# Optimization experiments

Measured on AMD Instinct MI355X. Metric: run time of the kernel, lower is better.

Reference implementation:

```python
import jax, jax.numpy as jnp
import numpy as np

B, S, D_MODEL = 2, 2048, 1024
H, D = 16, 64
D_INNER = H * D
EPS = 1e-5


def setup_inputs() -> dict:
    key = jax.random.key(0)
    ks = jax.random.split(key, 10)
    sc = 0.02
    return {
        "x": jax.random.normal(ks[0], (B, S, D_MODEL), dtype=jnp.float32),
        "Wq": jax.random.normal(ks[1], (D_MODEL, D_INNER), dtype=jnp.float32) * sc,
        "Wk": jax.random.normal(ks[2], (D_MODEL, D_INNER), dtype=jnp.float32) * sc,
        "Wv": jax.random.normal(ks[3], (D_MODEL, D_INNER), dtype=jnp.float32) * sc,
        "Wg": jax.random.normal(ks[4], (D_MODEL, D_INNER), dtype=jnp.float32) * sc,
        "Wa": jax.random.normal(ks[5], (D_MODEL, H), dtype=jnp.float32) * sc,
        "ba": jax.random.normal(ks[6], (H,), dtype=jnp.float32) * sc,
        "Wo": jax.random.normal(ks[7], (D_INNER, D_MODEL), dtype=jnp.float32) * sc,
        "gn_w": jnp.ones((D_INNER,), dtype=jnp.float32),
        "gn_b": jnp.zeros((D_INNER,), dtype=jnp.float32),
    }


def reference(x, Wq, Wk, Wv, Wg, Wa, ba, Wo, gn_w, gn_b):
    b, s, _ = x.shape
    # projections -> [B,H,S,D]
    q = jax.nn.silu(jnp.einsum('bsm,md->bsd', x, Wq).reshape(b, s, H, D).transpose(0, 2, 1, 3))
    k = jax.nn.silu(jnp.einsum('bsm,md->bsd', x, Wk).reshape(b, s, H, D).transpose(0, 2, 1, 3))
    v = jnp.einsum('bsm,md->bsd', x, Wv).reshape(b, s, H, D).transpose(0, 2, 1, 3)

    # data-dependent log forget gate, per head: [B,H,S]
    log_alpha = -jax.nn.softplus(jnp.einsum('bsm,mh->bsh', x, Wa) + ba)
    cum = jnp.cumsum(log_alpha, axis=1).transpose(0, 2, 1)  # [B,H,S]

    # decay[b,h,i,j] = exp(cum[i] - cum[j]) for j <= i, else 0
    diff = cum[:, :, :, None] - cum[:, :, None, :]  # [B,H,S,S]
    causal = jnp.tril(jnp.ones((s, s), dtype=bool))
    decay = jnp.exp(jnp.where(causal, diff, -jnp.inf))

    attn = jnp.einsum('bhid,bhjd->bhij', q, k) * decay
    o = jnp.einsum('bhij,bhjd->bhid', attn, v)  # [B,H,S,D]
    o = o.transpose(0, 2, 1, 3)  # [B,S,H,D]

    # GroupNorm(H groups) over channels-within-group and spatial dim S
    mean = jnp.mean(o, axis=(1, 3), keepdims=True)          # per (b,h)
    var = jnp.var(o, axis=(1, 3), keepdims=True)
    o = (o - mean) / jnp.sqrt(var + EPS)
    o = o * gn_w.reshape(H, D) + gn_b.reshape(H, D)
    o = o.reshape(b, s, H * D)

    gate = jax.nn.sigmoid(jnp.einsum('bsm,md->bsd', x, Wg))
    return jnp.einsum('bsd,dm->bsm', o * gate, Wo)
```

## Files before the change

### kernel.cpp

```cpp
#include <hip/hip_runtime.h>
#include <math.h>
#include <stdint.h>

typedef __attribute__((ext_vector_type(4))) float f32x4;
typedef __attribute__((ext_vector_type(8))) short bf16x8;

constexpr int NB = 2;
constexpr int NS = 2048;
constexpr int NM = 1024;
constexpr int NH = 16;
constexpr int ND = 64;
constexpr int NDI = 1024;

__device__ __forceinline__ float bf2f(unsigned short u) {
  uint32_t x = ((uint32_t)u) << 16; float f; __builtin_memcpy(&f, &x, 4); return f;
}
__device__ __forceinline__ unsigned short f2bf(float f) {
  uint32_t x; __builtin_memcpy(&x, &f, 4);
  x += 0x7FFFu + ((x >> 16) & 1u);
  return (unsigned short)(x >> 16);
}

__global__ __launch_bounds__(256) void k_prep(const float* __restrict__ x,
    const float* __restrict__ w0, const float* __restrict__ w1,
    const float* __restrict__ w2, const float* __restrict__ w3,
    const float* __restrict__ w4, const float* __restrict__ Wa,
    unsigned short* __restrict__ xb,
    unsigned short* __restrict__ t0, unsigned short* __restrict__ t1,
    unsigned short* __restrict__ t2, unsigned short* __restrict__ t3,
    unsigned short* __restrict__ t4, unsigned short* __restrict__ wa_pad) {
  int bid = blockIdx.x;
  if (bid < 2048) {
    int i = bid * 256 + threadIdx.x;
    const float4* p = (const float4*)(x + (size_t)i * 8);
    float4 a = p[0], b = p[1];
    unsigned short r[8] = {f2bf(a.x), f2bf(a.y), f2bf(a.z), f2bf(a.w),
                           f2bf(b.x), f2bf(b.y), f2bf(b.z), f2bf(b.w)};
    *(uint4*)(xb + (size_t)i * 8) = *(const uint4*)r;
  } else if (bid < 7168) {
    __shared__ float tile[32][33];
    int w = bid - 2048;
    int z = w >> 10, within = w & 1023;
    const float* src = z == 0 ? w0 : z == 1 ? w1 : z == 2 ? w2 : z == 3 ? w3 : w4;
    unsigned short* dst = z == 0 ? t0 : z == 1 ? t1 : z == 2 ? t2 : z == 3 ? t3 : t4;
    int c0 = (within & 31) * 32, r0 = (within >> 5) * 32;
    int tx = threadIdx.x & 31, ty = threadIdx.x >> 5;
    #pragma unroll
    for (int i = 0; i < 4; i++)
      tile[ty + i * 8][tx] = src[(size_t)(r0 + ty + i * 8) * 1024 + c0 + tx];
    __syncthreads();
    #pragma unroll
    for (int i = 0; i < 4; i++)
      dst[(size_t)(c0 + ty + i * 8) * 1024 + r0 + tx] = f2bf(tile[tx][ty + i * 8]);
  } else {
    int idx = (bid - 7168) * 256 + threadIdx.x;
    int h = idx >> 10, k2 = idx & 1023;
    wa_pad[idx] = (h < 16) ? f2bf(Wa[k2 * 16 + h]) : (unsigned short)0;
  }
}

__global__ __launch_bounds__(256) void k_la_gemm(const unsigned short* __restrict__ xb,
    const unsigned short* __restrict__ wa_pad, float* __restrict__ la4) {
  __shared__ unsigned short As[128 * 32];
  __shared__ unsigned short Bs[128 * 32];
  int tid = threadIdx.x;
  int row0 = blockIdx.y * 128;
  int kbeg = blockIdx.x * 256;
  float* Cp = la4 + (size_t)blockIdx.x * (32 * 2048);
  int w = tid >> 6, l = tid & 63;
  int wr = w >> 1, wc = w & 1;
  int lr = l & 15, lk = l >> 4;
  f32x4 acc[4] = {};
  for (int k0 = kbeg; k0 < kbeg + 256; k0 += 32) {
    __syncthreads();
    #pragma unroll
    for (int i = 0; i < 2; i++) {
      int idx = tid + i * 256;
      int r = idx >> 2, c = idx & 3;
      int cs = c ^ ((r >> 1) & 3);
      const unsigned short* srcA = xb + (size_t)(row0 + r) * NM + k0 + cs * 8;
      const unsigned short* srcB = wa_pad + (size_t)r * NM + k0 + cs * 8;
      __builtin_amdgcn_global_load_lds(
          (const __attribute__((address_space(1))) void*)srcA,
          (__attribute__((address_space(3))) void*)((char*)As + (w * 64 + i * 256) * 16),
          16, 0, 0);
      __builtin_amdgcn_global_load_lds(
          (const __attribute__((address_space(1))) void*)srcB,
          (__attribute__((address_space(3))) void*)((char*)Bs + (w * 64 + i * 256) * 16),
          16, 0, 0);
    }
    __syncthreads();
    if (wc == 0) {
      bf16x8 b = *(const bf16x8*)&Bs[lr * 32 + (lk ^ ((lr >> 1) & 3)) * 8];
      #pragma unroll
      for (int m = 0; m < 4; m++) {
        int ra = wr * 64 + m * 16 + lr;
        bf16x8 a = *(const bf16x8*)&As[ra * 32 + (lk ^ ((ra >> 1) & 3)) * 8];
        acc[m] = __builtin_amdgcn_mfma_f32_16x16x32_bf16(a, b, acc[m], 0, 0, 0);
      }
    }
  }
  if (wc == 0) {
    #pragma unroll
    for (int m = 0; m < 4; m++) {
      #pragma unroll
      for (int j = 0; j < 4; j++) {
        int row = row0 + wr * 64 + m * 16 + lk * 4 + j;
        int bb = row >> 11, s = row & 2047;
        Cp[((size_t)(bb * 16 + lr)) * 2048 + s] = acc[m][j];
      }
    }
  }
}

__global__ __launch_bounds__(256) void k_cumsum(const float* __restrict__ la4,
    const float* __restrict__ ba, float* __restrict__ cum,
    float* __restrict__ psum, float* __restrict__ psq) {
  int g = blockIdx.x;
  int h = g & 15;
  if (threadIdx.x == 0) { psum[g] = 0.f; psq[g] = 0.f; }
  float bah = ba[h];
  const float* p0 = la4 + (size_t)g * NS;
  float* out = cum + (size_t)g * NS;
  __shared__ float part[256];
  float v[8]; float sum = 0.f;
  int base = threadIdx.x * 8;
  #pragma unroll
  for (int i = 0; i < 8; i++) {
    int s = base + i;
    float z = p0[s] + p0[65536 + s] + p0[131072 + s] + p0[196608 + s] + bah;
    float sp = fmaxf(z, 0.f) + log1pf(expf(-fabsf(z)));
    v[i] = -sp; sum += v[i];
  }
  part[threadIdx.x] = sum;
  __syncthreads();
  for (int off = 1; off < 256; off <<= 1) {
    float add = (threadIdx.x >= off) ? part[threadIdx.x - off] : 0.f;
    __syncthreads();
    part[threadIdx.x] += add;
    __syncthreads();
  }
  float run = (threadIdx.x > 0) ? part[threadIdx.x - 1] : 0.f;
  #pragma unroll
  for (int i = 0; i < 8; i++) { run += v[i]; out[base + i] = run; }
}

#define LD8(base, r, kc) (*(const bf16x8*)((base) + (size_t)(r) * 128 + ((((kc)) ^ ((r) & 7)) * 16)))

__global__ __launch_bounds__(512, 1) void k_proj8(
    const unsigned short* __restrict__ A,
    const unsigned short* __restrict__ Wcat,
    unsigned short* __restrict__ q, unsigned short* __restrict__ k,
    unsigned short* __restrict__ v, unsigned short* __restrict__ g) {
  __shared__ unsigned short Ab[2][256 * 64];
  __shared__ unsigned short Bb[2][256 * 64];
  int tid = threadIdx.x;
  int bid = blockIdx.x;
  int wg = (bid & 7) * 32 + (bid >> 3);
  int bx = wg & 15, by = wg >> 4;
  int row0 = by * 256, col0 = bx * 256;
  int wid = tid >> 6, lane = tid & 63;
  int WR = wid >> 2, WC = wid & 3;
  int lr = lane & 15, lk = lane >> 4;

  auto stage = [&](int kt, int bi) {
    #pragma unroll
    for (int i = 0; i < 4; i++) {
      int idx = tid + i * 512;
      int r = idx >> 3, c = idx & 7;
      int cs = c ^ (r & 7);
      const unsigned short* srcA = A + (size_t)(row0 + r) * NM + kt * 64 + cs * 8;
      __builtin_amdgcn_global_load_lds(
          (const __attribute__((address_space(1))) void*)srcA,
          (__attribute__((address_space(3))) void*)((char*)&Ab[bi][0] + (wid * 64 + i * 512) * 16),
          16, 0, 0);
      const unsigned short* srcB = Wcat + (size_t)(col0 + r) * NM + kt * 64 + cs * 8;
      __builtin_amdgcn_global_load_lds(
          (const __attribute__((address_space(1))) void*)srcB,
          (__attribute__((address_space(3))) void*)((char*)&Bb[bi][0] + (wid * 64 + i * 512) * 16),
          16, 0, 0);
    }
  };

  stage(0, 0);
  stage(1, 1);

  f32x4 acc[8][4] = {};
  for (int kt = 0; kt < 16; ++kt) {
    int bi = kt & 1;
    if (kt < 15) asm volatile("s_waitcnt vmcnt(8)" ::: "memory");
    else         asm volatile("s_waitcnt vmcnt(0)" ::: "memory");
    __builtin_amdgcn_sched_barrier(0);
    __builtin_amdgcn_s_barrier();

    const char* Ap = (const char*)&Ab[bi][0];
    const char* Bp = (const char*)&Bb[bi][0];
    bf16x8 a[4][2], blo[2][2], bhi[2][2];
    #pragma unroll
    for (int m = 0; m < 4; m++) {
      int r = WR * 128 + m * 16 + lr;
      a[m][0] = LD8(Ap, r, lk); a[m][1] = LD8(Ap, r, lk + 4);
    }
    #pragma unroll
    for (int n = 0; n < 2; n++) {
      int r = WC * 64 + n * 16 + lr;
      blo[n][0] = LD8(Bp, r, lk); blo[n][1] = LD8(Bp, r, lk + 4);
    }
    __builtin_amdgcn_s_setprio(1);
    #pragma unroll
    for (int kk = 0; kk < 2; kk++)
      #pragma unroll
      for (int m = 0; m < 4; m++)
        #pragma unroll
        for (int n = 0; n < 2; n++)
          acc[m][n] = __builtin_amdgcn_mfma_f32_16x16x32_bf16(a[m][kk], blo[n][kk], acc[m][n], 0, 0, 0);
    __builtin_amdgcn_s_setprio(0);
    #pragma unroll
    for (int n = 0; n < 2; n++) {
      int r = WC * 64 + (2 + n) * 16 + lr;
      bhi[n][0] = LD8(Bp, r, lk); bhi[n][1] = LD8(Bp, r, lk + 4);
    }
    __builtin_amdgcn_s_barrier();
    __builtin_amdgcn_s_setprio(1);
    #pragma unroll
    for (int kk = 0; kk < 2; kk++)
      #pragma unroll
      for (int m = 0; m < 4; m++)
        #pragma unroll
        for (int n = 0; n < 2; n++)
          acc[m][2 + n] = __builtin_amdgcn_mfma_f32_16x16x32_bf16(a[m][kk], bhi[n][kk], acc[m][2 + n], 0, 0, 0);
    __builtin_amdgcn_s_setprio(0);
    #pragma unroll
    for (int m = 0; m < 4; m++) {
      int r = WR * 128 + (4 + m) * 16 + lr;
      a[m][0] = LD8(Ap, r, lk); a[m][1] = LD8(Ap, r, lk + 4);
    }
    __builtin_amdgcn_s_barrier();
    __builtin_amdgcn_s_setprio(1);
    #pragma unroll
    for (int kk = 0; kk < 2; kk++)
      #pragma unroll
      for (int m = 0; m < 4; m++)
        #pragma unroll
        for (int n = 0; n < 2; n++)
          acc[4 + m][2 + n] = __builtin_amdgcn_mfma_f32_16x16x32_bf16(a[m][kk], bhi[n][kk], acc[4 + m][2 + n], 0, 0, 0);
    __builtin_amdgcn_s_setprio(0);
    asm volatile("s_waitcnt lgkmcnt(0)" ::: "memory");
    __builtin_amdgcn_sched_barrier(0);
    __builtin_amdgcn_s_barrier();
    if (kt + 2 < 16) stage(kt + 2, bi);
    __builtin_amdgcn_s_setprio(1);
    #pragma unroll
    for (int kk = 0; kk < 2; kk++)
      #pragma unroll
      for (int m = 0; m < 4; m++)
        #pragma unroll
        for (int n = 0; n < 2; n++)
          acc[4 + m][n] = __builtin_amdgcn_mfma_f32_16x16x32_bf16(a[m][kk], blo[n][kk], acc[4 + m][n], 0, 0, 0);
    __builtin_amdgcn_s_setprio(0);
  }

  #pragma unroll
  for (int m = 0; m < 8; m++) {
    #pragma unroll
    for (int n = 0; n < 4; n++) {
      int col = col0 + WC * 64 + n * 16 + lr;
      int zone = col >> 10;
      unsigned short* dst = zone == 0 ? q : zone == 1 ? k : zone == 2 ? v : g;
      int cb = col & 1023;
      #pragma unroll
      for (int j = 0; j < 4; j++) {
        int row = row0 + WR * 128 + m * 16 + lk * 4 + j;
        float val = acc[m][n][j];
        if (zone <= 1) val = val / (1.f + expf(-val));
        else if (zone == 3) val = 1.f / (1.f + expf(-val));
        dst[(size_t)row * 1024 + cb] = f2bf(val);
      }
    }
  }
}

__global__ __launch_bounds__(256) void k_out2(const unsigned short* __restrict__ A,
    const unsigned short* __restrict__ Bt, float* __restrict__ C) {
  __shared__ unsigned short As[2][128 * 64];
  __shared__ unsigned short Bs[2][128 * 64];
  int tid = threadIdx.x;
  int bid = blockIdx.x;
  int wg = (bid & 7) * 32 + (bid >> 3);
  int bx = wg & 7, by = wg >> 3;
  int row0 = by * 128, col0 = bx * 128;
  int w = tid >> 6, l = tid & 63;
  int wr = w >> 1, wc = w & 1;
  int lr = l & 15, lk = l >> 4;

  auto stage = [&](int t, int bi) {
    #pragma unroll
    for (int i = 0; i < 4; i++) {
      int idx = tid + i * 256;
      int r = idx >> 3, c = idx & 7;
      int cs = c ^ (r & 7);
      const unsigned short* srcA = A + (size_t)(row0 + r) * NM + t * 64 + cs * 8;
      __builtin_amdgcn_global_load_lds(
          (const __attribute__((address_space(1))) void*)srcA,
          (__attribute__((address_space(3))) void*)((char*)&As[bi][0] + idx * 16),
          16, 0, 0);
      const unsigned short* srcB = Bt + (size_t)(col0 + r) * NM + t * 64 + cs * 8;
      __builtin_amdgcn_global_load_lds(
          (const __attribute__((address_space(1))) void*)srcB,
          (__attribute__((address_space(3))) void*)((char*)&Bs[bi][0] + idx * 16),
          16, 0, 0);
    }
  };

  stage(0, 0);
  asm volatile("s_waitcnt vmcnt(0)" ::: "memory");
  __builtin_amdgcn_s_barrier();

  f32x4 acc[4][4] = {};
  int cur = 0;
  for (int t = 0; t < 16; ++t) {
    if (t < 15) stage(t + 1, cur ^ 1);
    const char* Ap = (const char*)&As[cur][0];
    const char* Bp = (const char*)&Bs[cur][0];
    bf16x8 a[4][2], b[4][2];
    #pragma unroll
    for (int m = 0; m < 4; m++) {
      int ra = wr * 64 + m * 16 + lr;
      #pragma unroll
      for (int kk = 0; kk < 2; kk++)
        a[m][kk] = *(const bf16x8*)(Ap + ra * 128 + (((kk * 4 + lk) ^ (ra & 7)) * 16));
    }
    #pragma unroll
    for (int n = 0; n < 4; n++) {
      int rb = wc * 64 + n * 16 + lr;
      #pragma unroll
      for (int kk = 0; kk < 2; kk++)
        b[n][kk] = *(const bf16x8*)(Bp + rb * 128 + (((kk * 4 + lk) ^ (rb & 7)) * 16));
    }
    __builtin_amdgcn_s_setprio(1);
    #pragma unroll
    for (int kk = 0; kk < 2; kk++)
      #pragma unroll
      for (int m = 0; m < 4; m++)
        #pragma unroll
        for (int n = 0; n < 4; n++)
          acc[m][n] = __builtin_amdgcn_mfma_f32_16x16x32_bf16(a[m][kk], b[n][kk], acc[m][n], 0, 0, 0);
    __builtin_amdgcn_s_setprio(0);
    asm volatile("s_waitcnt vmcnt(0)" ::: "memory");
    __builtin_amdgcn_s_barrier();
    cur ^= 1;
  }
  #pragma unroll
  for (int m = 0; m < 4; m++)
    #pragma unroll
    for (int n = 0; n < 4; n++)
      #pragma unroll
      for (int j = 0; j < 4; j++) {
        int row = row0 + wr * 64 + m * 16 + lk * 4 + j;
        int col = col0 + wc * 64 + n * 16 + lr;
        C[(size_t)row * NM + col] = acc[m][n][j];
      }
}

__global__ __launch_bounds__(256) void k_attn(const unsigned short* __restrict__ q,
    const unsigned short* __restrict__ kk, const unsigned short* __restrict__ vv,
    const float* __restrict__ cum, unsigned short* __restrict__ o,
    float* __restrict__ psum, float* __restrict__ psq) {
  int it = blockIdx.x, h = blockIdx.y, b = blockIdx.z;
  int i0 = it * 64;
  __shared__ unsigned short Qs[64 * 64];
  __shared__ unsigned short Ks[64 * 64];
  __shared__ unsigned short Ps[64 * 64];
  __shared__ unsigned short Vs[64 * 66];
  __shared__ float ci[64], cj[64];
  __shared__ int jlo_s;
  int tid = threadIdx.x;
  int w = tid >> 6, lane = tid & 63;
  int cl = lane & 15, hi = lane >> 4;
  const size_t hb = (size_t)b * NS * NDI + (size_t)h * ND;
  const float* cumh = cum + (size_t)(b * NH + h) * NS;

  #pragma unroll
  for (int lp = 0; lp < 2; lp++) {
    int idx = tid + lp * 256;
    int r = idx >> 3, cb = (idx & 7) * 16;
    uint4 t = *(const uint4*)(q + hb + (size_t)(i0 + r) * NDI + (cb >> 1));
    *(uint4*)((char*)Qs + r * 128 + (cb ^ ((r & 7) << 4))) = t;
  }
  if (tid < 64) ci[tid] = cumh[i0 + tid];
  if (tid < 64) {
    int jt = tid;
    bool ok = (jt <= it) && (cumh[i0] - cumh[jt * 64 + 63] >= -60.f);
    unsigned long long mask = __ballot(ok);
    if (tid == 0) jlo_s = (int)__builtin_ctzll(mask);
  }
  __syncthreads();
  int jlo = jlo_s;

  int arow = w * 16 + cl;
  int xr = (cl & 7) << 4;
  const char* Qb = (const char*)Qs + arow * 128;
  const char* Pb = (const char*)Ps + arow * 128;
  f32x4 acco[4] = {};

  for (int jt = jlo; jt <= it; jt++) {
    int j0 = jt * 64;
    __syncthreads();
    if (tid < 64) cj[tid] = cumh[j0 + tid];
    __syncthreads();
    #pragma unroll
    for (int lp = 0; lp < 2; lp++) {
      int idx = tid + lp * 256;
      int r = idx >> 3, cb = (idx & 7) * 16;
      uint4 t = *(const uint4*)(kk + hb + (size_t)(j0 + r) * NDI + (cb >> 1));
      *(uint4*)((char*)Ks + r * 128 + (cb ^ ((r & 7) << 4))) = t;
      uint4 tv = *(const uint4*)(vv + hb + (size_t)(j0 + r) * NDI + (cb >> 1));
      unsigned int uv[4]; *(uint4*)uv = tv;
      unsigned int* vd = (unsigned int*)(Vs + r * 66 + (cb >> 1));
      vd[0] = uv[0]; vd[1] = uv[1]; vd[2] = uv[2]; vd[3] = uv[3];
    }
    __syncthreads();
    bf16x8 a0 = *(const bf16x8*)(Qb + ((hi * 16) ^ xr));
    bf16x8 a1 = *(const bf16x8*)(Qb + ((64 + hi * 16) ^ xr));
    f32x4 accs[4] = {};
    #pragma unroll
    for (int jtile = 0; jtile < 4; jtile++) {
      const char* Kb = (const char*)Ks + (jtile * 16 + cl) * 128;
      bf16x8 b0 = *(const bf16x8*)(Kb + ((hi * 16) ^ xr));
      bf16x8 b1 = *(const bf16x8*)(Kb + ((64 + hi * 16) ^ xr));
      accs[jtile] = __builtin_amdgcn_mfma_f32_16x16x32_bf16(a0, b0, accs[jtile], 0, 0, 0);
      accs[jtile] = __builtin_amdgcn_mfma_f32_16x16x32_bf16(a1, b1, accs[jtile], 0, 0, 0);
    }
    #pragma unroll
    for (int jtile = 0; jtile < 4; jtile++) {
      #pragma unroll
      for (int reg = 0; reg < 4; reg++) {
        int irl = w * 16 + hi * 4 + reg;
        int jl = jtile * 16 + cl;
        float dec = ((j0 + jl) <= (i0 + irl)) ? __expf(ci[irl] - cj[jl]) : 0.f;
        float pv = accs[jtile][reg] * dec;
        *(unsigned short*)((char*)Ps + irl * 128 + ((2 * jl) ^ ((irl & 7) << 4))) = f2bf(pv);
      }
    }
    __syncthreads();
    #pragma unroll
    for (int kk2 = 0; kk2 < 2; kk2++) {
      bf16x8 pa = *(const bf16x8*)(Pb + ((kk2 * 64 + hi * 16) ^ xr));
      #pragma unroll
      for (int dt = 0; dt < 4; dt++) {
        bf16x8 vb;
        #pragma unroll
        for (int e = 0; e < 8; e++)
          vb[e] = (short)Vs[(kk2 * 32 + hi * 8 + e) * 66 + dt * 16 + cl];
        acco[dt] = __builtin_amdgcn_mfma_f32_16x16x32_bf16(pa, vb, acco[dt], 0, 0, 0);
      }
    }
  }
  #pragma unroll
  for (int dt = 0; dt < 4; dt++) {
    #pragma unroll
    for (int reg = 0; reg < 4; reg++) {
      int row = i0 + w * 16 + hi * 4 + reg;
      o[hb + (size_t)row * NDI + dt * 16 + cl] = f2bf(acco[dt][reg]);
    }
  }
  __syncthreads();
  float* ls = (float*)Ps;
  float* lq = ls + 256;
  float sm = 0.f, sq = 0.f;
  #pragma unroll
  for (int dt = 0; dt < 4; dt++)
    #pragma unroll
    for (int reg = 0; reg < 4; reg++) { float t2 = acco[dt][reg]; sm += t2; sq += t2 * t2; }
  ls[tid] = sm; lq[tid] = sq;
  __syncthreads();
  for (int off = 128; off > 0; off >>= 1) {
    if (tid < off) { ls[tid] += ls[tid + off]; lq[tid] += lq[tid + off]; }
    __syncthreads();
  }
  if (tid == 0) {
    atomicAdd(&psum[b * NH + h], ls[0]);
    atomicAdd(&psq[b * NH + h], lq[0]);
  }
}

__global__ __launch_bounds__(256) void k_gate(const unsigned short* __restrict__ o,
    const unsigned short* __restrict__ gsig, const float* __restrict__ psum,
    const float* __restrict__ psq, const float* __restrict__ gnw,
    const float* __restrict__ gnb, unsigned short* __restrict__ u) {
  int idx4 = blockIdx.x * 256 + threadIdx.x;
  size_t base = (size_t)idx4 * 4;
  int c = (int)(base & (NDI - 1));
  int row = (int)(base >> 10);
  int b = row >> 11;
  int h = c >> 6;
  int g = b * NH + h;
  float n = (float)(NS * ND);
  float mean = psum[g] / n;
  float var = psq[g] / n - mean * mean;
  float rstd = rsqrtf(var + 1e-5f);
  ushort4 ov = *(const ushort4*)(o + base);
  ushort4 gv = *(const ushort4*)(gsig + base);
  float4 w4 = *(const float4*)(gnw + c);
  float4 b4 = *(const float4*)(gnb + c);
  unsigned short r[4];
  r[0] = f2bf(((bf2f(ov.x) - mean) * rstd * w4.x + b4.x) * bf2f(gv.x));
  r[1] = f2bf(((bf2f(ov.y) - mean) * rstd * w4.y + b4.y) * bf2f(gv.y));
  r[2] = f2bf(((bf2f(ov.z) - mean) * rstd * w4.z + b4.z) * bf2f(gv.z));
  r[3] = f2bf(((bf2f(ov.w) - mean) * rstd * w4.w + b4.w) * bf2f(gv.w));
  *(ushort4*)(u + base) = *(const ushort4*)r;
}

extern "C" void kernel_launch(void* const* d_in, const int* in_sizes, int n_in,
                              void* d_out, int out_size, void* d_ws, size_t ws_size,
                              hipStream_t stream) {
  const float* x   = (const float*)d_in[0];
  const float* Wq  = (const float*)d_in[1];
  const float* Wk  = (const float*)d_in[2];
  const float* Wv  = (const float*)d_in[3];
  const float* Wg  = (const float*)d_in[4];
  const float* Wa  = (const float*)d_in[5];
  const float* ba  = (const float*)d_in[6];
  const float* Wo  = (const float*)d_in[7];
  const float* gnw = (const float*)d_in[8];
  const float* gnb = (const float*)d_in[9];
  float* out = (float*)d_out;

  const size_t NTOK = (size_t)NB * NS;
  char* p = (char*)d_ws;
  float* la4 = (float*)p;                 p += (size_t)4 * 32 * NS * 4;
  float* cum = (float*)p;                 p += (size_t)NB * NH * NS * 4;
  float* psum = (float*)p;                p += 32 * 4;
  float* psq  = (float*)p;                p += 32 * 4;
  p = (char*)(((uintptr_t)p + 255) & ~(uintptr_t)255);
  unsigned short* xb   = (unsigned short*)p; p += NTOK * NM * 2;
  unsigned short* Wcat = (unsigned short*)p; p += (size_t)4 * NM * NDI * 2;
  unsigned short* wto  = (unsigned short*)p; p += (size_t)NDI * NM * 2;
  unsigned short* wa_pad = (unsigned short*)p; p += (size_t)128 * NM * 2;
  unsigned short* q  = (unsigned short*)p;  p += NTOK * NDI * 2;
  unsigned short* k  = (unsigned short*)p;  p += NTOK * NDI * 2;
  unsigned short* v  = (unsigned short*)p;  p += NTOK * NDI * 2;
  unsigned short* g  = (unsigned short*)p;  p += NTOK * NDI * 2;
  unsigned short* u  = (unsigned short*)p;  p += NTOK * NDI * 2;
  unsigned short* o  = (unsigned short*)p;  p += NTOK * NDI * 2;

  unsigned short* wtq = Wcat;
  unsigned short* wtk = Wcat + (size_t)NM * NDI;
  unsigned short* wtv = Wcat + (size_t)2 * NM * NDI;
  unsigned short* wtg = Wcat + (size_t)3 * NM * NDI;

  k_prep    <<<dim3(7680), 256, 0, stream>>>(x, Wq, Wk, Wv, Wg, Wo, Wa,
                                             xb, wtq, wtk, wtv, wtg, wto, wa_pad);
  k_la_gemm <<<dim3(4, 32), 256, 0, stream>>>(xb, wa_pad, la4);
  k_cumsum  <<<dim3(NB * NH), 256, 0, stream>>>(la4, ba, cum, psum, psq);
  k_proj8   <<<dim3(256), 512, 0, stream>>>(xb, Wcat, q, k, v, g);
  k_attn    <<<dim3(32, NH, NB), 256, 0, stream>>>(q, k, v, cum, o, psum, psq);
  k_gate    <<<dim3(4096), 256, 0, stream>>>(o, g, psum, psq, gnw, gnb, u);
  k_out2    <<<dim3(256), 256, 0, stream>>>(u, wto, out);
}
```

Baseline: 126.3 us.

## Fuse forget-gate projection into QKVG GEMM and switch to 128x128 tiles

The separate log-alpha GEMM and its 4-way split-K partial buffer are removed. The padded Wa block is appended as an extra 128-column tile of the concatenated weight, and the softplus epilogue moves into the projection GEMM, so cumsum only does the prefix scan. The hand-pipelined 256x256, 512-thread projection kernel is replaced by a simpler 128x128, 256-thread double-buffered kernel over 1056 blocks, which saves one launch. The trade is a less tuned GEMM inner loop and lower per-block reuse, and the extra Wa tile wastes compute on padding columns.

```diff
diff --git a/kernel.cpp b/kernel.cpp
--- a/kernel.cpp
+++ b/kernel.cpp
@@ -59,79 +59,17 @@
   }
 }
 
-__global__ __launch_bounds__(256) void k_la_gemm(const unsigned short* __restrict__ xb,
-    const unsigned short* __restrict__ wa_pad, float* __restrict__ la4) {
-  __shared__ unsigned short As[128 * 32];
-  __shared__ unsigned short Bs[128 * 32];
-  int tid = threadIdx.x;
-  int row0 = blockIdx.y * 128;
-  int kbeg = blockIdx.x * 256;
-  float* Cp = la4 + (size_t)blockIdx.x * (32 * 2048);
-  int w = tid >> 6, l = tid & 63;
-  int wr = w >> 1, wc = w & 1;
-  int lr = l & 15, lk = l >> 4;
-  f32x4 acc[4] = {};
-  for (int k0 = kbeg; k0 < kbeg + 256; k0 += 32) {
-    __syncthreads();
-    #pragma unroll
-    for (int i = 0; i < 2; i++) {
-      int idx = tid + i * 256;
-      int r = idx >> 2, c = idx & 3;
-      int cs = c ^ ((r >> 1) & 3);
-      const unsigned short* srcA = xb + (size_t)(row0 + r) * NM + k0 + cs * 8;
-      const unsigned short* srcB = wa_pad + (size_t)r * NM + k0 + cs * 8;
-      __builtin_amdgcn_global_load_lds(
-          (const __attribute__((address_space(1))) void*)srcA,
-          (__attribute__((address_space(3))) void*)((char*)As + (w * 64 + i * 256) * 16),
-          16, 0, 0);
-      __builtin_amdgcn_global_load_lds(
-          (const __attribute__((address_space(1))) void*)srcB,
-          (__attribute__((address_space(3))) void*)((char*)Bs + (w * 64 + i * 256) * 16),
-          16, 0, 0);
-    }
-    __syncthreads();
-    if (wc == 0) {
-      bf16x8 b = *(const bf16x8*)&Bs[lr * 32 + (lk ^ ((lr >> 1) & 3)) * 8];
-      #pragma unroll
-      for (int m = 0; m < 4; m++) {
-        int ra = wr * 64 + m * 16 + lr;
-        bf16x8 a = *(const bf16x8*)&As[ra * 32 + (lk ^ ((ra >> 1) & 3)) * 8];
-        acc[m] = __builtin_amdgcn_mfma_f32_16x16x32_bf16(a, b, acc[m], 0, 0, 0);
-      }
-    }
-  }
-  if (wc == 0) {
-    #pragma unroll
-    for (int m = 0; m < 4; m++) {
-      #pragma unroll
-      for (int j = 0; j < 4; j++) {
-        int row = row0 + wr * 64 + m * 16 + lk * 4 + j;
-        int bb = row >> 11, s = row & 2047;
-        Cp[((size_t)(bb * 16 + lr)) * 2048 + s] = acc[m][j];
-      }
-    }
-  }
-}
-
-__global__ __launch_bounds__(256) void k_cumsum(const float* __restrict__ la4,
-    const float* __restrict__ ba, float* __restrict__ cum,
-    float* __restrict__ psum, float* __restrict__ psq) {
+__global__ __launch_bounds__(256) void k_cumsum(const float* __restrict__ la,
+    float* __restrict__ cum, float* __restrict__ psum, float* __restrict__ psq) {
   int g = blockIdx.x;
-  int h = g & 15;
   if (threadIdx.x == 0) { psum[g] = 0.f; psq[g] = 0.f; }
-  float bah = ba[h];
-  const float* p0 = la4 + (size_t)g * NS;
+  const float* p0 = la + (size_t)g * NS;
   float* out = cum + (size_t)g * NS;
   __shared__ float part[256];
   float v[8]; float sum = 0.f;
   int base = threadIdx.x * 8;
   #pragma unroll
-  for (int i = 0; i < 8; i++) {
-    int s = base + i;
-    float z = p0[s] + p0[65536 + s] + p0[131072 + s] + p0[196608 + s] + bah;
-    float sp = fmaxf(z, 0.f) + log1pf(expf(-fabsf(z)));
-    v[i] = -sp; sum += v[i];
-  }
+  for (int i = 0; i < 8; i++) { v[i] = p0[base + i]; sum += v[i]; }
   part[threadIdx.x] = sum;
   __syncthreads();
   for (int off = 1; off < 256; off <<= 1) {
@@ -145,66 +83,65 @@
   for (int i = 0; i < 8; i++) { run += v[i]; out[base + i] = run; }
 }
 
-#define LD8(base, r, kc) (*(const bf16x8*)((base) + (size_t)(r) * 128 + ((((kc)) ^ ((r) & 7)) * 16)))
-
-__global__ __launch_bounds__(512, 1) void k_proj8(
-    const unsigned short* __restrict__ A,
-    const unsigned short* __restrict__ Wcat,
+__global__ __launch_bounds__(256) void k_proj2(const unsigned short* __restrict__ A,
+    const unsigned short* __restrict__ Bt, const float* __restrict__ ba,
     unsigned short* __restrict__ q, unsigned short* __restrict__ k,
-    unsigned short* __restrict__ v, unsigned short* __restrict__ g) {
-  __shared__ unsigned short Ab[2][256 * 64];
-  __shared__ unsigned short Bb[2][256 * 64];
+    unsigned short* __restrict__ v, unsigned short* __restrict__ g,
+    float* __restrict__ la) {
+  __shared__ unsigned short As[2][128 * 64];
+  __shared__ unsigned short Bs[2][128 * 64];
   int tid = threadIdx.x;
   int bid = blockIdx.x;
-  int wg = (bid & 7) * 32 + (bid >> 3);
-  int bx = wg & 15, by = wg >> 4;
-  int row0 = by * 256, col0 = bx * 256;
-  int wid = tid >> 6, lane = tid & 63;
-  int WR = wid >> 2, WC = wid & 3;
-  int lr = lane & 15, lk = lane >> 4;
-
-  auto stage = [&](int kt, int bi) {
+  int wg = (bid & 7) * 132 + (bid >> 3);
+  int by = wg & 31, bx = wg >> 5;
+  int row0 = by * 128, col0 = bx * 128;
+  int w = tid >> 6, l = tid & 63;
+  int wr = w >> 1, wc = w & 1;
+  int lr = l & 15, lk = l >> 4;
+
+  auto stage = [&](int t, int bi) {
     #pragma unroll
     for (int i = 0; i < 4; i++) {
-      int idx = tid + i * 512;
+      int idx = tid + i * 256;
       int r = idx >> 3, c = idx & 7;
       int cs = c ^ (r & 7);
-      const unsigned short* srcA = A + (size_t)(row0 + r) * NM + kt * 64 + cs * 8;
+      const unsigned short* srcA = A + (size_t)(row0 + r) * NM + t * 64 + cs * 8;
       __builtin_amdgcn_global_load_lds(
           (const __attribute__((address_space(1))) void*)srcA,
-          (__attribute__((address_space(3))) void*)((char*)&Ab[bi][0] + (wid * 64 + i * 512) * 16),
+          (__attribute__((address_space(3))) void*)((char*)&As[bi][0] + idx * 16),
           16, 0, 0);
-      const unsigned short* srcB = Wcat + (size_t)(col0 + r) * NM + kt * 64 + cs * 8;
+      const unsigned short* srcB = Bt + (size_t)(col0 + r) * NM + t * 64 + cs * 8;
       __builtin_amdgcn_global_load_lds(
           (const __attribute__((address_space(1))) void*)srcB,
-          (__attribute__((address_space(3))) void*)((char*)&Bb[bi][0] + (wid * 64 + i * 512) * 16),
+          (__attribute__((address_space(3))) void*)((char*)&Bs[bi][0] + idx * 16),
           16, 0, 0);
     }
   };
 
   stage(0, 0);
-  stage(1, 1);
-
-  f32x4 acc[8][4] = {};
-  for (int kt = 0; kt < 16; ++kt) {
-    int bi = kt & 1;
-    if (kt < 15) asm volatile("s_waitcnt vmcnt(8)" ::: "memory");
-    else         asm volatile("s_waitcnt vmcnt(0)" ::: "memory");
-    __builtin_amdgcn_sched_barrier(0);
-    __builtin_amdgcn_s_barrier();
-
-    const char* Ap = (const char*)&Ab[bi][0];
-    const char* Bp = (const char*)&Bb[bi][0];
-    bf16x8 a[4][2], blo[2][2], bhi[2][2];
+  asm volatile("s_waitcnt vmcnt(0)" ::: "memory");
+  __builtin_amdgcn_s_barrier();
+
+  f32x4 acc[4][4] = {};
+  int cur = 0;
+  for (int t = 0; t < 16; ++t) {
+    if (t < 15) stage(t + 1, cur ^ 1);
+    const char* Ap = (const char*)&As[cur][0];
+    const char* Bp = (const char*)&Bs[cur][0];
+    bf16x8 a[4][2], b[4][2];
     #pragma unroll
     for (int m = 0; m < 4; m++) {
-      int r = WR * 128 + m * 16 + lr;
-      a[m][0] = LD8(Ap, r, lk); a[m][1] = LD8(Ap, r, lk + 4);
-    }
-    #pragma unroll
-    for (int n = 0; n < 2; n++) {
-      int r = WC * 64 + n * 16 + lr;
-      blo[n][0] = LD8(Bp, r, lk); blo[n][1] = LD8(Bp, r, lk + 4);
+      int ra = wr * 64 + m * 16 + lr;
+      #pragma unroll
+      for (int kk = 0; kk < 2; kk++)
+        a[m][kk] = *(const bf16x8*)(Ap + ra * 128 + (((kk * 4 + lk) ^ (ra & 7)) * 16));
+    }
+    #pragma unroll
+    for (int n = 0; n < 4; n++) {
+      int rb = wc * 64 + n * 16 + lr;
+      #pragma unroll
+      for (int kk = 0; kk < 2; kk++)
+        b[n][kk] = *(const bf16x8*)(Bp + rb * 128 + (((kk * 4 + lk) ^ (rb & 7)) * 16));
     }
     __builtin_amdgcn_s_setprio(1);
     #pragma unroll
@@ -212,65 +149,42 @@
       #pragma unroll
       for (int m = 0; m < 4; m++)
         #pragma unroll
-        for (int n = 0; n < 2; n++)
-          acc[m][n] = __builtin_amdgcn_mfma_f32_16x16x32_bf16(a[m][kk], blo[n][kk], acc[m][n], 0, 0, 0);
+        for (int n = 0; n < 4; n++)
+          acc[m][n] = __builtin_amdgcn_mfma_f32_16x16x32_bf16(a[m][kk], b[n][kk], acc[m][n], 0, 0, 0);
     __builtin_amdgcn_s_setprio(0);
-    #pragma unroll
-    for (int n = 0; n < 2; n++) {
-      int r = WC * 64 + (2 + n) * 16 + lr;
-      bhi[n][0] = LD8(Bp, r, lk); bhi[n][1] = LD8(Bp, r, lk + 4);
-    }
+    asm volatile("s_waitcnt vmcnt(0)" ::: "memory");
     __builtin_amdgcn_s_barrier();
-    __builtin_amdgcn_s_setprio(1);
-    #pragma unroll
-    for (int kk = 0; kk < 2; kk++)
-      #pragma unroll
-      for (int m = 0; m < 4; m++)
+    cur ^= 1;
+  }
+
+  if (col0 >= 4096) {
+    if (wc == 0) {
+      float bah = ba[lr];
+      #pragma unroll
+      for (int m = 0; m < 4; m++) {
         #pragma unroll
-        for (int n = 0; n < 2; n++)
-          acc[m][2 + n] = __builtin_amdgcn_mfma_f32_16x16x32_bf16(a[m][kk], bhi[n][kk], acc[m][2 + n], 0, 0, 0);
-    __builtin_amdgcn_s_setprio(0);
-    #pragma unroll
-    for (int m = 0; m < 4; m++) {
-      int r = WR * 128 + (4 + m) * 16 + lr;
-      a[m][0] = LD8(Ap, r, lk); a[m][1] = LD8(Ap, r, lk + 4);
-    }
-    __builtin_amdgcn_s_barrier();
-    __builtin_amdgcn_s_setprio(1);
-    #pragma unroll
-    for (int kk = 0; kk < 2; kk++)
-      #pragma unroll
-      for (int m = 0; m < 4; m++)
-        #pragma unroll
-        for (int n = 0; n < 2; n++)
-          acc[4 + m][2 + n] = __builtin_amdgcn_mfma_f32_16x16x32_bf16(a[m][kk], bhi[n][kk], acc[4 + m][2 + n], 0, 0, 0);
-    __builtin_amdgcn_s_setprio(0);
-    asm volatile("s_waitcnt lgkmcnt(0)" ::: "memory");
-    __builtin_amdgcn_sched_barrier(0);
-    __builtin_amdgcn_s_barrier();
-    if (kt + 2 < 16) stage(kt + 2, bi);
-    __builtin_amdgcn_s_setprio(1);
-    #pragma unroll
-    for (int kk = 0; kk < 2; kk++)
-      #pragma unroll
-      for (int m = 0; m < 4; m++)
-        #pragma unroll
-        for (int n = 0; n < 2; n++)
-          acc[4 + m][n] = __builtin_amdgcn_mfma_f32_16x16x32_bf16(a[m][kk], blo[n][kk], acc[4 + m][n], 0, 0, 0);
-    __builtin_amdgcn_s_setprio(0);
-  }
-
-  #pragma unroll
-  for (int m = 0; m < 8; m++) {
+        for (int j = 0; j < 4; j++) {
+          int row = row0 + wr * 64 + m * 16 + lk * 4 + j;
+          float z = acc[m][0][j] + bah;
+          float sp = fmaxf(z, 0.f) + log1pf(expf(-fabsf(z)));
+          int bb = row >> 11, s = row & 2047;
+          la[((size_t)(bb * 16 + lr)) * 2048 + s] = -sp;
+        }
+      }
+    }
+    return;
+  }
+  #pragma unroll
+  for (int m = 0; m < 4; m++) {
     #pragma unroll
     for (int n = 0; n < 4; n++) {
-      int col = col0 + WC * 64 + n * 16 + lr;
+      int col = col0 + wc * 64 + n * 16 + lr;
       int zone = col >> 10;
       unsigned short* dst = zone == 0 ? q : zone == 1 ? k : zone == 2 ? v : g;
       int cb = col & 1023;
       #pragma unroll
       for (int j = 0; j < 4; j++) {
-        int row = row0 + WR * 128 + m * 16 + lk * 4 + j;
+        int row = row0 + wr * 64 + m * 16 + lk * 4 + j;
         float val = acc[m][n][j];
         if (zone <= 1) val = val / (1.f + expf(-val));
         else if (zone == 3) val = 1.f / (1.f + expf(-val));
@@ -528,15 +442,14 @@
 
   const size_t NTOK = (size_t)NB * NS;
   char* p = (char*)d_ws;
-  float* la4 = (float*)p;                 p += (size_t)4 * 32 * NS * 4;
+  float* la  = (float*)p;                 p += (size_t)NB * NH * NS * 4;
   float* cum = (float*)p;                 p += (size_t)NB * NH * NS * 4;
   float* psum = (float*)p;                p += 32 * 4;
   float* psq  = (float*)p;                p += 32 * 4;
   p = (char*)(((uintptr_t)p + 255) & ~(uintptr_t)255);
-  unsigned short* xb   = (unsigned short*)p; p += NTOK * NM * 2;
-  unsigned short* Wcat = (unsigned short*)p; p += (size_t)4 * NM * NDI * 2;
-  unsigned short* wto  = (unsigned short*)p; p += (size_t)NDI * NM * 2;
-  unsigned short* wa_pad = (unsigned short*)p; p += (size_t)128 * NM * 2;
+  unsigned short* xb    = (unsigned short*)p; p += NTOK * NM * 2;
+  unsigned short* Wcat5 = (unsigned short*)p; p += (size_t)4224 * NM * 2;
+  unsigned short* wto   = (unsigned short*)p; p += (size_t)NDI * NM * 2;
   unsigned short* q  = (unsigned short*)p;  p += NTOK * NDI * 2;
   unsigned short* k  = (unsigned short*)p;  p += NTOK * NDI * 2;
   unsigned short* v  = (unsigned short*)p;  p += NTOK * NDI * 2;
@@ -544,17 +457,17 @@
   unsigned short* u  = (unsigned short*)p;  p += NTOK * NDI * 2;
   unsigned short* o  = (unsigned short*)p;  p += NTOK * NDI * 2;
 
-  unsigned short* wtq = Wcat;
-  unsigned short* wtk = Wcat + (size_t)NM * NDI;
-  unsigned short* wtv = Wcat + (size_t)2 * NM * NDI;
-  unsigned short* wtg = Wcat + (size_t)3 * NM * NDI;
-
-  k_prep    <<<dim3(7680), 256, 0, stream>>>(x, Wq, Wk, Wv, Wg, Wo, Wa,
-                                             xb, wtq, wtk, wtv, wtg, wto, wa_pad);
-  k_la_gemm <<<dim3(4, 32), 256, 0, stream>>>(xb, wa_pad, la4);
-  k_cumsum  <<<dim3(NB * NH), 256, 0, stream>>>(la4, ba, cum, psum, psq);
-  k_proj8   <<<dim3(256), 512, 0, stream>>>(xb, Wcat, q, k, v, g);
-  k_attn    <<<dim3(32, NH, NB), 256, 0, stream>>>(q, k, v, cum, o, psum, psq);
-  k_gate    <<<dim3(4096), 256, 0, stream>>>(o, g, psum, psq, gnw, gnb, u);
-  k_out2    <<<dim3(256), 256, 0, stream>>>(u, wto, out);
-}
+  unsigned short* wtq = Wcat5;
+  unsigned short* wtk = Wcat5 + (size_t)NM * NDI;
+  unsigned short* wtv = Wcat5 + (size_t)2 * NM * NDI;
+  unsigned short* wtg = Wcat5 + (size_t)3 * NM * NDI;
+  unsigned short* wa_pad = Wcat5 + (size_t)4 * NM * NDI;
+
+  k_prep   <<<dim3(7680), 256, 0, stream>>>(x, Wq, Wk, Wv, Wg, Wo, Wa,
+                                            xb, wtq, wtk, wtv, wtg, wto, wa_pad);
+  k_proj2  <<<dim3(1056), 256, 0, stream>>>(xb, Wcat5, ba, q, k, v, g, la);
+  k_cumsum <<<dim3(NB * NH), 256, 0, stream>>>(la, cum, psum, psq);
+  k_attn   <<<dim3(32, NH, NB), 256, 0, stream>>>(q, k, v, cum, o, psum, psq);
+  k_gate   <<<dim3(4096), 256, 0, stream>>>(o, g, psum, psq, gnw, gnb, u);
+  k_out2   <<<dim3(256), 256, 0, stream>>>(u, wto, out);
+}
```

New measurement: 152.1 us. 1.2x slower.
